# Optimization experiments

Hardware: AMD Instinct MI355X
Metric: run time of the kernel (lower is better)

Reference implementation:

```python
import jax, jax.numpy as jnp
import numpy as np

# e2m1 FP4 value table: sign bit in nibble MSB, values {0,0.5,1,1.5,2,3,4,6}
_E2M1 = jnp.array([0.0, 0.5, 1.0, 1.5, 2.0, 3.0, 4.0, 6.0,
                   -0.0, -0.5, -1.0, -1.5, -2.0, -3.0, -4.0, -6.0], dtype=jnp.float32)


def _dequant_fp4(packed, scales, group_size):
    """packed: [E, out, in//8] uint32; scales: [E, in//group_size, out] -> [E, out, in] f32."""
    shifts = jnp.arange(8, dtype=jnp.uint32) * 4  # nibble shift amounts 0,4,...,28
    nib = (packed[..., None] >> shifts) & jnp.uint32(0xF)  # [E, out, in//8, 8]
    E, O, P, _ = nib.shape
    nib = nib.reshape(E, O, P * 8).astype(jnp.int32)
    w = _E2M1[nib]  # [E, out, in] f32
    gids = jnp.arange(P * 8) // group_size  # group id per input column
    sc = jnp.transpose(scales, (0, 2, 1))[:, :, gids]  # [E, out, in]
    return w * sc


def setup_inputs() -> dict:
    E, H, I, T, K, G = 8, 2048, 1408, 2048, 2, 128
    key = jax.random.key(0)
    ks = jax.random.split(key, 9)
    x = jax.random.normal(ks[0], (T, H), dtype=jnp.float32)
    gate_packed = jax.random.bits(ks[1], (E, I, H // 8), dtype=jnp.uint32)
    up_packed = jax.random.bits(ks[2], (E, I, H // 8), dtype=jnp.uint32)
    down_packed = jax.random.bits(ks[3], (E, H, I // 8), dtype=jnp.uint32)
    gate_scales = jax.random.uniform(ks[4], (E, H // G, I), jnp.float32, 0.5, 1.5)
    up_scales = jax.random.uniform(ks[5], (E, H // G, I), jnp.float32, 0.5, 1.5)
    down_scales = jax.random.uniform(ks[6], (E, I // G, H), jnp.float32, 0.5, 1.5)
    topk_idx = jax.random.randint(ks[7], (T, K), 0, E, dtype=jnp.int32)
    w = jax.random.uniform(ks[8], (T, K), jnp.float32)
    topk_w = w / jnp.sum(w, axis=-1, keepdims=True)
    return {"x": x,
            "gate_packed": gate_packed, "gate_scales": gate_scales,
            "up_packed": up_packed, "up_scales": up_scales,
            "down_packed": down_packed, "down_scales": down_scales,
            "topk_idx": topk_idx, "topk_w": topk_w, "group_size": G}


def reference(x, gate_packed, gate_scales, up_packed, up_scales,
              down_packed, down_scales, topk_idx, topk_w, group_size):
    # Fused dequant (nibble unpack + e2m1 table + per-group scale) for all experts
    gate_w = _dequant_fp4(gate_packed, gate_scales, group_size)  # [E, I, H]
    up_w = _dequant_fp4(up_packed, up_scales, group_size)        # [E, I, H]
    down_w = _dequant_fp4(down_packed, down_scales, group_size)  # [E, H, I]
    # Grouped SwiGLU expert MLP (dense over E=8 experts, gather routed outputs)
    g = jnp.einsum('th,eih->eti', x, gate_w)
    u = jnp.einsum('th,eih->eti', x, up_w)
    h = jax.nn.silu(g) * u                                        # [E, T, I]
    y = jnp.einsum('eti,ehi->eth', h, down_w)                     # [E, T, H]
    T = x.shape[0]
    sel = y[topk_idx, jnp.arange(T)[:, None], :]                  # [T, K, H]
    return jnp.sum(sel * topk_w[..., None], axis=1)               # [T, H]
```

## Files before the change

### kernel.cpp

```cpp
#include <hip/hip_runtime.h>
#include <hip/hip_bf16.h>
#include <stdint.h>

#define E_ 8
#define H_ 2048
#define I_ 1408
#define T_ 2048
#define K_ 2
#define G_ 128

typedef __bf16 bf16;
typedef bf16 bf16x8 __attribute__((ext_vector_type(8)));
typedef float f32x4 __attribute__((ext_vector_type(4)));

__device__ __forceinline__ uint32_t prm(uint32_t hi, uint32_t lo, uint32_t sel) {
    return __builtin_amdgcn_perm(hi, lo, sel);
}

struct DequantTab { uint32_t thi0, thi1, tlo0, tlo1; };

__device__ __forceinline__ DequantTab build_tab(float s) {
    union { bf16 h[8]; uint32_t u[4]; } tb;
    tb.h[0] = (bf16)(0.0f);
    tb.h[1] = (bf16)(0.5f * s);
    tb.h[2] = (bf16)(1.0f * s);
    tb.h[3] = (bf16)(1.5f * s);
    tb.h[4] = (bf16)(2.0f * s);
    tb.h[5] = (bf16)(3.0f * s);
    tb.h[6] = (bf16)(4.0f * s);
    tb.h[7] = (bf16)(6.0f * s);
    DequantTab t;
    t.thi0 = prm(tb.u[1], tb.u[0], 0x07050301u);
    t.tlo0 = prm(tb.u[1], tb.u[0], 0x06040200u);
    t.thi1 = prm(tb.u[3], tb.u[2], 0x07050301u);
    t.tlo1 = prm(tb.u[3], tb.u[2], 0x06040200u);
    return t;
}

__device__ __forceinline__ uint4 dequant8t(uint32_t p, const DequantTab& t) {
    const uint32_t pr = p >> 4;
    const uint32_t pe = p  & 0x07070707u;
    const uint32_t po = pr & 0x07070707u;
    const uint32_t He = prm(t.thi1, t.thi0, pe) | ((p  & 0x08080808u) << 4);
    const uint32_t Le = prm(t.tlo1, t.tlo0, pe);
    const uint32_t Ho = prm(t.thi1, t.thi0, po) | ((pr & 0x08080808u) << 4);
    const uint32_t Lo = prm(t.tlo1, t.tlo0, po);
    const uint32_t E01 = prm(He, Le, 0x05010400u);
    const uint32_t E23 = prm(He, Le, 0x07030602u);
    const uint32_t O01 = prm(Ho, Lo, 0x05010400u);
    const uint32_t O23 = prm(Ho, Lo, 0x07030602u);
    return make_uint4(prm(O01, E01, 0x05040100u),
                      prm(O01, E01, 0x07060302u),
                      prm(O23, E23, 0x05040100u),
                      prm(O23, E23, 0x07060302u));
}

__device__ __forceinline__ void gld16(void* lds, const void* g) {
    __builtin_amdgcn_global_load_lds(
        (__attribute__((address_space(1))) void*)g,
        (__attribute__((address_space(3))) void*)lds, 16, 0, 0);
}

__global__ void route_count(const int* __restrict__ topk_idx, int* __restrict__ counts) {
    int p = blockIdx.x * blockDim.x + threadIdx.x;
    if (p < T_ * K_) atomicAdd(&counts[topk_idx[p]], 1);
}

__global__ void route_scan(const int* __restrict__ counts, int* __restrict__ offsets,
                           int* __restrict__ tmap) {
    if (threadIdx.x == 0) {
        int acc = 0, ti = 0;
        for (int e = 0; e < E_; e++) {
            offsets[e] = acc;
            int nt = (counts[e] + 63) >> 6;
            for (int j = 0; j < nt; j++) tmap[ti++] = (e << 16) | j;
            acc += counts[e];
        }
        offsets[E_] = acc;
        for (; ti < 128; ti++) tmap[ti] = -1;
    }
}

__global__ void route_fill(const int* __restrict__ topk_idx, const float* __restrict__ topk_w,
                           int* __restrict__ cursors, const int* __restrict__ offsets,
                           int* __restrict__ tok, float* __restrict__ wgt,
                           int* __restrict__ inv) {
    int p = blockIdx.x * blockDim.x + threadIdx.x;
    if (p < T_ * K_) {
        int e = topk_idx[p];
        int slot = atomicAdd(&cursors[e], 1);
        int idx = offsets[e] + slot;
        tok[idx] = p / K_;
        wgt[idx] = topk_w[p];
        inv[p] = idx;
    }
}

__global__ __launch_bounds__(256)
void xcast_kernel(const float* __restrict__ x, uint4* __restrict__ xb) {
    const int i = blockIdx.x * 256 + threadIdx.x;
    const float4 a = ((const float4*)x)[i * 2];
    const float4 b = ((const float4*)x)[i * 2 + 1];
    union { uint4 u; bf16 h[8]; } r;
    r.h[0] = (bf16)a.x; r.h[1] = (bf16)a.y; r.h[2] = (bf16)a.z; r.h[3] = (bf16)a.w;
    r.h[4] = (bf16)b.x; r.h[5] = (bf16)b.y; r.h[6] = (bf16)b.z; r.h[7] = (bf16)b.w;
    xb[i] = r.u;
}

__global__ __launch_bounds__(256, 4)
void gemm1t_kernel(const bf16* __restrict__ xb,
                   const uint32_t* __restrict__ gate_packed,
                   const float* __restrict__ gate_scales,
                   const uint32_t* __restrict__ up_packed,
                   const float* __restrict__ up_scales,
                   const int* __restrict__ offsets,
                   const int* __restrict__ tmap,
                   const int* __restrict__ tok, bf16* __restrict__ h_buf)
{
    const int tm = tmap[blockIdx.x];
    if (tm < 0) return;
    const int e = tm >> 16, ty = tm & 0xffff;
    const int row0 = offsets[e];
    const int cnt = offsets[e + 1] - row0;
    const int itile = blockIdx.y;

    __shared__ __align__(16) bf16 xs[64][64];
    __shared__ __align__(16) bf16 wgs[64][64];
    __shared__ __align__(16) bf16 wus[64][64];

    const int tid = threadIdx.x;

    const int xr0 = tid >> 3;
    const int xr1 = xr0 + 32;
    const int xc  = tid & 7;
    int g0 = ty * 64 + xr0;  g0 = (g0 < cnt) ? g0 : (cnt - 1);
    int g1 = ty * 64 + xr1;  g1 = (g1 < cnt) ? g1 : (cnt - 1);
    const bf16* xsrc0 = xb + (size_t)tok[row0 + g0] * H_ + ((xc ^ (xr0 & 7)) * 8);
    const bf16* xsrc1 = xb + (size_t)tok[row0 + g1] * H_ + ((xc ^ (xr1 & 7)) * 8);
    bf16* xdst0 = &xs[xr0][xc * 8];
    bf16* xdst1 = &xs[xr1][xc * 8];

    const int mat  = tid >> 7;
    const int id   = tid & 127;
    const int wrow = id >> 1;
    const int quad = id & 1;
    const int irow = itile * 64 + wrow;
    const uint32_t* wp_row = (mat ? up_packed : gate_packed)
        + (size_t)e * I_ * (H_ / 8) + (size_t)irow * (H_ / 8) + quad * 4;
    const float* ws_row = (mat ? up_scales : gate_scales)
        + (size_t)e * (H_ / G_) * I_ + irow;
    bf16 (* const wdst)[64] = mat ? wus : wgs;

    const int wave = tid >> 6, lane = tid & 63;
    const int wy = wave >> 1, wx = wave & 1;
    const int lrow = lane & 15, kq = lane >> 4;

    f32x4 accg[2][2] = {};
    f32x4 accu[2][2] = {};

    for (int kg = 0; kg < H_ / G_; kg++) {
        const DequantTab tw = build_tab(ws_row[kg * I_]);
#pragma unroll
        for (int kh2 = 0; kh2 < 2; kh2++) {
            const int k0 = kg * 128 + kh2 * 64;
            gld16(xdst0, xsrc0 + k0);
            gld16(xdst1, xsrc1 + k0);
            const uint4 pw = *(const uint4*)(wp_row + (k0 >> 3));
            {
                uint4 d0 = dequant8t(pw.x, tw);
                uint4 d1 = dequant8t(pw.y, tw);
                uint4 d2 = dequant8t(pw.z, tw);
                uint4 d3 = dequant8t(pw.w, tw);
                const int cb = quad * 4, rs = wrow & 7;
                *(uint4*)&wdst[wrow][((cb + 0) ^ rs) * 8] = d0;
                *(uint4*)&wdst[wrow][((cb + 1) ^ rs) * 8] = d1;
                *(uint4*)&wdst[wrow][((cb + 2) ^ rs) * 8] = d2;
                *(uint4*)&wdst[wrow][((cb + 3) ^ rs) * 8] = d3;
            }
            __syncthreads();

#pragma unroll
            for (int kh = 0; kh < 2; kh++) {
                bf16x8 a[2], bg[2], bu[2];
#pragma unroll
                for (int mi = 0; mi < 2; mi++) {
                    const int ra = wy * 32 + mi * 16 + lrow;
                    a[mi] = *(const bf16x8*)&xs[ra][((kh * 4 + kq) ^ (ra & 7)) * 8];
                }
#pragma unroll
                for (int ni = 0; ni < 2; ni++) {
                    const int rb = wx * 32 + ni * 16 + lrow;
                    const int cb = ((kh * 4 + kq) ^ (rb & 7)) * 8;
                    bg[ni] = *(const bf16x8*)&wgs[rb][cb];
                    bu[ni] = *(const bf16x8*)&wus[rb][cb];
                }
#pragma unroll
                for (int mi = 0; mi < 2; mi++)
#pragma unroll
                    for (int ni = 0; ni < 2; ni++) {
                        accg[mi][ni] = __builtin_amdgcn_mfma_f32_16x16x32_bf16(a[mi], bg[ni], accg[mi][ni], 0, 0, 0);
                        accu[mi][ni] = __builtin_amdgcn_mfma_f32_16x16x32_bf16(a[mi], bu[ni], accu[mi][ni], 0, 0, 0);
                    }
            }
            __syncthreads();
        }
    }

#pragma unroll
    for (int mi = 0; mi < 2; mi++)
#pragma unroll
        for (int ni = 0; ni < 2; ni++) {
            const int icol = itile * 64 + wx * 32 + ni * 16 + lrow;
#pragma unroll
            for (int r = 0; r < 4; r++) {
                const int grow = ty * 64 + wy * 32 + mi * 16 + kq * 4 + r;
                if (grow < cnt) {
                    const float gv = accg[mi][ni][r];
                    const float hv = gv / (1.f + __expf(-gv)) * accu[mi][ni][r];
                    h_buf[(size_t)(row0 + grow) * I_ + icol] = (bf16)hv;
                }
            }
        }
}

__global__ __launch_bounds__(256, 4)
void gemm2t_kernel(const bf16* __restrict__ h_buf,
                   const uint32_t* __restrict__ down_packed,
                   const float* __restrict__ down_scales,
                   const int* __restrict__ offsets,
                   const int* __restrict__ tmap,
                   const float* __restrict__ wgt, float* __restrict__ yp)
{
    const int tm = tmap[blockIdx.x];
    if (tm < 0) return;
    const int e = tm >> 16, ty = tm & 0xffff;
    const int row0 = offsets[e];
    const int cnt = offsets[e + 1] - row0;
    const int htile = blockIdx.y;

    __shared__ __align__(16) bf16 hs[64][64];
    __shared__ __align__(16) bf16 wds[128][64];

    const int tid = threadIdx.x;

    const int xr0 = tid >> 3;
    const int xr1 = xr0 + 32;
    const int xc  = tid & 7;
    int g0 = ty * 64 + xr0;  g0 = (g0 < cnt) ? g0 : (cnt - 1);
    int g1 = ty * 64 + xr1;  g1 = (g1 < cnt) ? g1 : (cnt - 1);
    const bf16* hsrc0 = h_buf + (size_t)(row0 + g0) * I_ + ((xc ^ (xr0 & 7)) * 8);
    const bf16* hsrc1 = h_buf + (size_t)(row0 + g1) * I_ + ((xc ^ (xr1 & 7)) * 8);
    bf16* hdst0 = &hs[xr0][xc * 8];
    bf16* hdst1 = &hs[xr1][xc * 8];

    const int wrow = tid >> 1;
    const int quad = tid & 1;
    const int hrow = htile * 128 + wrow;
    const uint32_t* dp_row = down_packed + (size_t)e * H_ * (I_ / 8) + (size_t)hrow * (I_ / 8) + quad * 4;
    const float* ds_row = down_scales + (size_t)e * (I_ / G_) * H_ + hrow;

    const int wave = tid >> 6, lane = tid & 63;
    const int wy = wave >> 1, wx = wave & 1;
    const int lrow = lane & 15, kq = lane >> 4;

    f32x4 acc[2][4] = {};

    for (int kg = 0; kg < I_ / G_; kg++) {
        const DequantTab td = build_tab(ds_row[kg * H_]);
#pragma unroll
        for (int kh2 = 0; kh2 < 2; kh2++) {
            const int k0 = kg * 128 + kh2 * 64;
            gld16(hdst0, hsrc0 + k0);
            gld16(hdst1, hsrc1 + k0);
            const uint4 pw = *(const uint4*)(dp_row + (k0 >> 3));
            {
                uint4 d0 = dequant8t(pw.x, td);
                uint4 d1 = dequant8t(pw.y, td);
                uint4 d2 = dequant8t(pw.z, td);
                uint4 d3 = dequant8t(pw.w, td);
                const int cb = quad * 4, rs = wrow & 7;
                *(uint4*)&wds[wrow][((cb + 0) ^ rs) * 8] = d0;
                *(uint4*)&wds[wrow][((cb + 1) ^ rs) * 8] = d1;
                *(uint4*)&wds[wrow][((cb + 2) ^ rs) * 8] = d2;
                *(uint4*)&wds[wrow][((cb + 3) ^ rs) * 8] = d3;
            }
            __syncthreads();

#pragma unroll
            for (int kh = 0; kh < 2; kh++) {
                bf16x8 a[2], b[4];
#pragma unroll
                for (int mi = 0; mi < 2; mi++) {
                    const int ra = wy * 32 + mi * 16 + lrow;
                    a[mi] = *(const bf16x8*)&hs[ra][((kh * 4 + kq) ^ (ra & 7)) * 8];
                }
#pragma unroll
                for (int ni = 0; ni < 4; ni++) {
                    const int rb = wx * 64 + ni * 16 + lrow;
                    b[ni] = *(const bf16x8*)&wds[rb][((kh * 4 + kq) ^ (rb & 7)) * 8];
                }
#pragma unroll
                for (int mi = 0; mi < 2; mi++)
#pragma unroll
                    for (int ni = 0; ni < 4; ni++)
                        acc[mi][ni] = __builtin_amdgcn_mfma_f32_16x16x32_bf16(a[mi], b[ni], acc[mi][ni], 0, 0, 0);
            }
            __syncthreads();
        }
    }

#pragma unroll
    for (int mi = 0; mi < 2; mi++)
#pragma unroll
        for (int r = 0; r < 4; r++) {
            const int lr = wy * 32 + mi * 16 + kq * 4 + r;
            const int grow = ty * 64 + lr;
            if (grow < cnt) {
                const float w = wgt[row0 + grow];
#pragma unroll
                for (int ni = 0; ni < 4; ni++) {
                    const int col = htile * 128 + wx * 64 + ni * 16 + lrow;
                    yp[(size_t)(row0 + grow) * H_ + col] = acc[mi][ni][r] * w;
                }
            }
        }
}

__global__ __launch_bounds__(256)
void combine_kernel(const float* __restrict__ yp, const int* __restrict__ inv,
                    float* __restrict__ out) {
    const int idx = blockIdx.x * 256 + threadIdx.x;
    const int t = idx >> 9;
    const int c = idx & 511;
    const float4 a = ((const float4*)yp)[(size_t)inv[t * 2] * (H_ / 4) + c];
    const float4 b = ((const float4*)yp)[(size_t)inv[t * 2 + 1] * (H_ / 4) + c];
    float4 o;
    o.x = a.x + b.x; o.y = a.y + b.y; o.z = a.z + b.z; o.w = a.w + b.w;
    ((float4*)out)[idx] = o;
}

extern "C" void kernel_launch(void* const* d_in, const int* in_sizes, int n_in,
                              void* d_out, int out_size, void* d_ws, size_t ws_size,
                              hipStream_t stream) {
    const float* x = (const float*)d_in[0];
    const uint32_t* gate_packed = (const uint32_t*)d_in[1];
    const float* gate_scales = (const float*)d_in[2];
    const uint32_t* up_packed = (const uint32_t*)d_in[3];
    const float* up_scales = (const float*)d_in[4];
    const uint32_t* down_packed = (const uint32_t*)d_in[5];
    const float* down_scales = (const float*)d_in[6];
    const int* topk_idx = (const int*)d_in[7];
    const float* topk_w = (const float*)d_in[8];
    float* out = (float*)d_out;

    char* ws = (char*)d_ws;
    int* counts  = (int*)ws;
    int* cursors = (int*)(ws + 32);
    int* offsets = (int*)(ws + 64);
    int* tmap    = (int*)(ws + 128);
    int* tok     = (int*)(ws + 640);
    float* wgt   = (float*)(ws + 17024);
    int* inv     = (int*)(ws + 33408);
    bf16* h_buf  = (bf16*)(ws + 49792);
    bf16* xb     = (bf16*)(ws + 49792 + 11534336ull);
    float* yp    = (float*)(ws + 49792 + 11534336ull + 8388608ull);

    hipMemsetAsync(d_ws, 0, 1024, stream);

    route_count<<<(T_ * K_ + 255) / 256, 256, 0, stream>>>(topk_idx, counts);
    route_scan<<<1, 64, 0, stream>>>(counts, offsets, tmap);
    route_fill<<<(T_ * K_ + 255) / 256, 256, 0, stream>>>(topk_idx, topk_w, cursors, offsets,
                                                          tok, wgt, inv);
    xcast_kernel<<<T_ * H_ / 8 / 256, 256, 0, stream>>>(x, (uint4*)xb);

    dim3 g1(72, I_ / 64);
    gemm1t_kernel<<<g1, 256, 0, stream>>>(xb, gate_packed, gate_scales, up_packed, up_scales,
                                          offsets, tmap, tok, h_buf);
    dim3 g2(72, H_ / 128);
    gemm2t_kernel<<<g2, 256, 0, stream>>>(h_buf, down_packed, down_scales,
                                          offsets, tmap, wgt, yp);
    combine_kernel<<<T_ * H_ / 4 / 256, 256, 0, stream>>>(yp, inv, out);
}
```

Before: 286.5 us.

## Double-buffer activation tiles and grow token tile to 128 rows

```diff
diff --git a/kernel.cpp b/kernel.cpp
--- a/kernel.cpp
+++ b/kernel.cpp
@@ -72,12 +72,12 @@
         int acc = 0, ti = 0;
         for (int e = 0; e < E_; e++) {
             offsets[e] = acc;
-            int nt = (counts[e] + 63) >> 6;
+            int nt = (counts[e] + 127) >> 7;
             for (int j = 0; j < nt; j++) tmap[ti++] = (e << 16) | j;
             acc += counts[e];
         }
         offsets[E_] = acc;
-        for (; ti < 128; ti++) tmap[ti] = -1;
+        for (; ti < 64; ti++) tmap[ti] = -1;
     }
 }
 
@@ -107,7 +107,7 @@
     xb[i] = r.u;
 }
 
-__global__ __launch_bounds__(256, 4)
+__global__ __launch_bounds__(256, 3)
 void gemm1t_kernel(const bf16* __restrict__ xb,
                    const uint32_t* __restrict__ gate_packed,
                    const float* __restrict__ gate_scales,
@@ -124,21 +124,24 @@
     const int cnt = offsets[e + 1] - row0;
     const int itile = blockIdx.y;
 
-    __shared__ __align__(16) bf16 xs[64][64];
+    __shared__ __align__(16) bf16 xs[2][128][64];
     __shared__ __align__(16) bf16 wgs[64][64];
     __shared__ __align__(16) bf16 wus[64][64];
 
     const int tid = threadIdx.x;
 
-    const int xr0 = tid >> 3;
-    const int xr1 = xr0 + 32;
-    const int xc  = tid & 7;
-    int g0 = ty * 64 + xr0;  g0 = (g0 < cnt) ? g0 : (cnt - 1);
-    int g1 = ty * 64 + xr1;  g1 = (g1 < cnt) ? g1 : (cnt - 1);
-    const bf16* xsrc0 = xb + (size_t)tok[row0 + g0] * H_ + ((xc ^ (xr0 & 7)) * 8);
-    const bf16* xsrc1 = xb + (size_t)tok[row0 + g1] * H_ + ((xc ^ (xr1 & 7)) * 8);
-    bf16* xdst0 = &xs[xr0][xc * 8];
-    bf16* xdst1 = &xs[xr1][xc * 8];
+    const int xr = tid >> 3;
+    const int xc = tid & 7;
+    const int xch = (xc ^ (xr & 7)) * 8;
+    const bf16* xsrc[4];
+    bf16* xdst[4];
+#pragma unroll
+    for (int j = 0; j < 4; ++j) {
+        int g = ty * 128 + xr + j * 32;
+        g = (g < cnt) ? g : (cnt - 1);
+        xsrc[j] = xb + (size_t)tok[row0 + g] * H_ + xch;
+        xdst[j] = &xs[0][xr + j * 32][xc * 8];
+    }
 
     const int mat  = tid >> 7;
     const int id   = tid & 127;
@@ -155,17 +158,29 @@
     const int wy = wave >> 1, wx = wave & 1;
     const int lrow = lane & 15, kq = lane >> 4;
 
-    f32x4 accg[2][2] = {};
-    f32x4 accu[2][2] = {};
-
-    for (int kg = 0; kg < H_ / G_; kg++) {
-        const DequantTab tw = build_tab(ws_row[kg * I_]);
-#pragma unroll
-        for (int kh2 = 0; kh2 < 2; kh2++) {
-            const int k0 = kg * 128 + kh2 * 64;
-            gld16(xdst0, xsrc0 + k0);
-            gld16(xdst1, xsrc1 + k0);
-            const uint4 pw = *(const uint4*)(wp_row + (k0 >> 3));
+    f32x4 accg[4][2] = {};
+    f32x4 accu[4][2] = {};
+
+    float sc_cur = ws_row[0];
+    uint4 pw = *(const uint4*)(wp_row);
+#pragma unroll
+    for (int j = 0; j < 4; ++j) gld16(xdst[j], xsrc[j]);
+
+    constexpr int NG = H_ / G_;
+    constexpr int NT = 2 * NG;
+    for (int kg = 0; kg < NG; ++kg) {
+        const int kgn = (kg + 1 < NG) ? kg + 1 : kg;
+        const float sc_nxt = ws_row[(size_t)kgn * I_];
+        const DequantTab tw = build_tab(sc_cur);
+#pragma unroll
+        for (int kh2 = 0; kh2 < 2; ++kh2) {
+            const int t  = kg * 2 + kh2;
+            const int tn = (t < NT - 1) ? t + 1 : t;
+            const uint4 pwn = *(const uint4*)(wp_row + tn * 8);
+#pragma unroll
+            for (int j = 0; j < 4; ++j)
+                gld16(xdst[j] + (kh2 ^ 1) * (128 * 64), xsrc[j] + tn * 64);
+            __builtin_amdgcn_sched_barrier(0);
             {
                 uint4 d0 = dequant8t(pw.x, tw);
                 uint4 d1 = dequant8t(pw.y, tw);
@@ -177,43 +192,50 @@
                 *(uint4*)&wdst[wrow][((cb + 2) ^ rs) * 8] = d2;
                 *(uint4*)&wdst[wrow][((cb + 3) ^ rs) * 8] = d3;
             }
-            __syncthreads();
-
-#pragma unroll
-            for (int kh = 0; kh < 2; kh++) {
-                bf16x8 a[2], bg[2], bu[2];
-#pragma unroll
-                for (int mi = 0; mi < 2; mi++) {
-                    const int ra = wy * 32 + mi * 16 + lrow;
-                    a[mi] = *(const bf16x8*)&xs[ra][((kh * 4 + kq) ^ (ra & 7)) * 8];
-                }
-#pragma unroll
-                for (int ni = 0; ni < 2; ni++) {
+            __builtin_amdgcn_sched_barrier(0);
+            if (kh2 == 0) asm volatile("s_waitcnt vmcnt(6) lgkmcnt(0)" ::: "memory");
+            else          asm volatile("s_waitcnt vmcnt(5) lgkmcnt(0)" ::: "memory");
+            __builtin_amdgcn_s_barrier();
+            __builtin_amdgcn_sched_barrier(0);
+#pragma unroll
+            for (int kh = 0; kh < 2; ++kh) {
+                bf16x8 a[4], bg[2], bu[2];
+#pragma unroll
+                for (int mi = 0; mi < 4; ++mi) {
+                    const int ra = wy * 64 + mi * 16 + lrow;
+                    a[mi] = *(const bf16x8*)&xs[kh2][ra][((kh * 4 + kq) ^ (ra & 7)) * 8];
+                }
+#pragma unroll
+                for (int ni = 0; ni < 2; ++ni) {
                     const int rb = wx * 32 + ni * 16 + lrow;
-                    const int cb = ((kh * 4 + kq) ^ (rb & 7)) * 8;
-                    bg[ni] = *(const bf16x8*)&wgs[rb][cb];
-                    bu[ni] = *(const bf16x8*)&wus[rb][cb];
-                }
-#pragma unroll
-                for (int mi = 0; mi < 2; mi++)
-#pragma unroll
-                    for (int ni = 0; ni < 2; ni++) {
+                    const int cb2 = ((kh * 4 + kq) ^ (rb & 7)) * 8;
+                    bg[ni] = *(const bf16x8*)&wgs[rb][cb2];
+                    bu[ni] = *(const bf16x8*)&wus[rb][cb2];
+                }
+#pragma unroll
+                for (int mi = 0; mi < 4; ++mi)
+#pragma unroll
+                    for (int ni = 0; ni < 2; ++ni) {
                         accg[mi][ni] = __builtin_amdgcn_mfma_f32_16x16x32_bf16(a[mi], bg[ni], accg[mi][ni], 0, 0, 0);
                         accu[mi][ni] = __builtin_amdgcn_mfma_f32_16x16x32_bf16(a[mi], bu[ni], accu[mi][ni], 0, 0, 0);
                     }
             }
-            __syncthreads();
+            __builtin_amdgcn_sched_barrier(0);
+            asm volatile("s_waitcnt lgkmcnt(0)" ::: "memory");
+            __builtin_amdgcn_s_barrier();
+            pw = pwn;
         }
-    }
-
-#pragma unroll
-    for (int mi = 0; mi < 2; mi++)
-#pragma unroll
-        for (int ni = 0; ni < 2; ni++) {
+        sc_cur = sc_nxt;
+    }
+
+#pragma unroll
+    for (int mi = 0; mi < 4; ++mi)
+#pragma unroll
+        for (int ni = 0; ni < 2; ++ni) {
             const int icol = itile * 64 + wx * 32 + ni * 16 + lrow;
 #pragma unroll
-            for (int r = 0; r < 4; r++) {
-                const int grow = ty * 64 + wy * 32 + mi * 16 + kq * 4 + r;
+            for (int r = 0; r < 4; ++r) {
+                const int grow = ty * 128 + wy * 64 + mi * 16 + kq * 4 + r;
                 if (grow < cnt) {
                     const float gv = accg[mi][ni][r];
                     const float hv = gv / (1.f + __expf(-gv)) * accu[mi][ni][r];
@@ -223,7 +245,7 @@
         }
 }
 
-__global__ __launch_bounds__(256, 4)
+__global__ __launch_bounds__(256, 3)
 void gemm2t_kernel(const bf16* __restrict__ h_buf,
                    const uint32_t* __restrict__ down_packed,
                    const float* __restrict__ down_scales,
@@ -238,20 +260,23 @@
     const int cnt = offsets[e + 1] - row0;
     const int htile = blockIdx.y;
 
-    __shared__ __align__(16) bf16 hs[64][64];
+    __shared__ __align__(16) bf16 hs[2][128][64];
     __shared__ __align__(16) bf16 wds[128][64];
 
     const int tid = threadIdx.x;
 
-    const int xr0 = tid >> 3;
-    const int xr1 = xr0 + 32;
-    const int xc  = tid & 7;
-    int g0 = ty * 64 + xr0;  g0 = (g0 < cnt) ? g0 : (cnt - 1);
-    int g1 = ty * 64 + xr1;  g1 = (g1 < cnt) ? g1 : (cnt - 1);
-    const bf16* hsrc0 = h_buf + (size_t)(row0 + g0) * I_ + ((xc ^ (xr0 & 7)) * 8);
-    const bf16* hsrc1 = h_buf + (size_t)(row0 + g1) * I_ + ((xc ^ (xr1 & 7)) * 8);
-    bf16* hdst0 = &hs[xr0][xc * 8];
-    bf16* hdst1 = &hs[xr1][xc * 8];
+    const int xr = tid >> 3;
+    const int xc = tid & 7;
+    const int xch = (xc ^ (xr & 7)) * 8;
+    const bf16* hsrc[4];
+    bf16* hdst[4];
+#pragma unroll
+    for (int j = 0; j < 4; ++j) {
+        int g = ty * 128 + xr + j * 32;
+        g = (g < cnt) ? g : (cnt - 1);
+        hsrc[j] = h_buf + (size_t)(row0 + g) * I_ + xch;
+        hdst[j] = &hs[0][xr + j * 32][xc * 8];
+    }
 
     const int wrow = tid >> 1;
     const int quad = tid & 1;
@@ -263,16 +288,28 @@
     const int wy = wave >> 1, wx = wave & 1;
     const int lrow = lane & 15, kq = lane >> 4;
 
-    f32x4 acc[2][4] = {};
-
-    for (int kg = 0; kg < I_ / G_; kg++) {
-        const DequantTab td = build_tab(ds_row[kg * H_]);
-#pragma unroll
-        for (int kh2 = 0; kh2 < 2; kh2++) {
-            const int k0 = kg * 128 + kh2 * 64;
-            gld16(hdst0, hsrc0 + k0);
-            gld16(hdst1, hsrc1 + k0);
-            const uint4 pw = *(const uint4*)(dp_row + (k0 >> 3));
+    f32x4 acc[4][4] = {};
+
+    float sc_cur = ds_row[0];
+    uint4 pw = *(const uint4*)(dp_row);
+#pragma unroll
+    for (int j = 0; j < 4; ++j) gld16(hdst[j], hsrc[j]);
+
+    constexpr int NG = I_ / G_;
+    constexpr int NT = 2 * NG;
+    for (int kg = 0; kg < NG; ++kg) {
+        const int kgn = (kg + 1 < NG) ? kg + 1 : kg;
+        const float sc_nxt = ds_row[(size_t)kgn * H_];
+        const DequantTab td = build_tab(sc_cur);
+#pragma unroll
+        for (int kh2 = 0; kh2 < 2; ++kh2) {
+            const int t  = kg * 2 + kh2;
+            const int tn = (t < NT - 1) ? t + 1 : t;
+            const uint4 pwn = *(const uint4*)(dp_row + tn * 8);
+#pragma unroll
+            for (int j = 0; j < 4; ++j)
+                gld16(hdst[j] + (kh2 ^ 1) * (128 * 64), hsrc[j] + tn * 64);
+            __builtin_amdgcn_sched_barrier(0);
             {
                 uint4 d0 = dequant8t(pw.x, td);
                 uint4 d1 = dequant8t(pw.y, td);
@@ -284,41 +321,47 @@
                 *(uint4*)&wds[wrow][((cb + 2) ^ rs) * 8] = d2;
                 *(uint4*)&wds[wrow][((cb + 3) ^ rs) * 8] = d3;
             }
-            __syncthreads();
-
-#pragma unroll
-            for (int kh = 0; kh < 2; kh++) {
-                bf16x8 a[2], b[4];
-#pragma unroll
-                for (int mi = 0; mi < 2; mi++) {
-                    const int ra = wy * 32 + mi * 16 + lrow;
-                    a[mi] = *(const bf16x8*)&hs[ra][((kh * 4 + kq) ^ (ra & 7)) * 8];
-                }
-#pragma unroll
-                for (int ni = 0; ni < 4; ni++) {
+            __builtin_amdgcn_sched_barrier(0);
+            if (kh2 == 0) asm volatile("s_waitcnt vmcnt(6) lgkmcnt(0)" ::: "memory");
+            else          asm volatile("s_waitcnt vmcnt(5) lgkmcnt(0)" ::: "memory");
+            __builtin_amdgcn_s_barrier();
+            __builtin_amdgcn_sched_barrier(0);
+#pragma unroll
+            for (int kh = 0; kh < 2; ++kh) {
+                bf16x8 a[4], b[4];
+#pragma unroll
+                for (int mi = 0; mi < 4; ++mi) {
+                    const int ra = wy * 64 + mi * 16 + lrow;
+                    a[mi] = *(const bf16x8*)&hs[kh2][ra][((kh * 4 + kq) ^ (ra & 7)) * 8];
+                }
+#pragma unroll
+                for (int ni = 0; ni < 4; ++ni) {
                     const int rb = wx * 64 + ni * 16 + lrow;
                     b[ni] = *(const bf16x8*)&wds[rb][((kh * 4 + kq) ^ (rb & 7)) * 8];
                 }
 #pragma unroll
-                for (int mi = 0; mi < 2; mi++)
-#pragma unroll
-                    for (int ni = 0; ni < 4; ni++)
+                for (int mi = 0; mi < 4; ++mi)
+#pragma unroll
+                    for (int ni = 0; ni < 4; ++ni)
                         acc[mi][ni] = __builtin_amdgcn_mfma_f32_16x16x32_bf16(a[mi], b[ni], acc[mi][ni], 0, 0, 0);
             }
-            __syncthreads();
+            __builtin_amdgcn_sched_barrier(0);
+            asm volatile("s_waitcnt lgkmcnt(0)" ::: "memory");
+            __builtin_amdgcn_s_barrier();
+            pw = pwn;
         }
-    }
-
-#pragma unroll
-    for (int mi = 0; mi < 2; mi++)
-#pragma unroll
-        for (int r = 0; r < 4; r++) {
-            const int lr = wy * 32 + mi * 16 + kq * 4 + r;
-            const int grow = ty * 64 + lr;
+        sc_cur = sc_nxt;
+    }
+
+#pragma unroll
+    for (int mi = 0; mi < 4; ++mi)
+#pragma unroll
+        for (int r = 0; r < 4; ++r) {
+            const int grow = ty * 128 + wy * 64 + mi * 16 + kq * 4 + r;
             if (grow < cnt) {
                 const float w = wgt[row0 + grow];
 #pragma unroll
-                for (int ni = 0; ni < 4; ni++) {
+                for (int ni = 0; ni < 4; ++ni) {
                     const int col = htile * 128 + wx * 64 + ni * 16 + lrow;
                     yp[(size_t)(row0 + grow) * H_ + col] = acc[mi][ni][r] * w;
                 }
@@ -373,10 +416,10 @@
                                                           tok, wgt, inv);
     xcast_kernel<<<T_ * H_ / 8 / 256, 256, 0, stream>>>(x, (uint4*)xb);
 
-    dim3 g1(72, I_ / 64);
+    dim3 g1(40, I_ / 64);
     gemm1t_kernel<<<g1, 256, 0, stream>>>(xb, gate_packed, gate_scales, up_packed, up_scales,
                                           offsets, tmap, tok, h_buf);
-    dim3 g2(72, H_ / 128);
+    dim3 g2(40, H_ / 128);
     gemm2t_kernel<<<g2, 256, 0, stream>>>(h_buf, down_packed, down_scales,
                                           offsets, tmap, wgt, yp);
     combine_kernel<<<T_ * H_ / 4 / 256, 256, 0, stream>>>(yp, inv, out);
```

Result: faster. 271.6 us (-5.2%).
